# Performance work log

Hardware: AMD Instinct MI355X
Metric: run time of the kernel (lower is better)

## Reference

```python
import jax, jax.numpy as jnp
import numpy as np

B, N, D, H = 2, 2048, 512, 8
HD = D // H
EPS = 1e-5


def layernorm(x, g, b):
    m = jnp.mean(x, axis=-1, keepdims=True)
    v = jnp.var(x, axis=-1, keepdims=True)
    return (x - m) * jax.lax.rsqrt(v + EPS) * g + b


def setup_inputs() -> dict:
    key = jax.random.key(0)
    ks = jax.random.split(key, 16)
    s = 1.0 / np.sqrt(D)
    def lin(k, din, dout):
        k1, k2 = jax.random.split(k)
        return (jax.random.uniform(k1, (din, dout), jnp.float32, -s, s),
                jax.random.uniform(k2, (dout,), jnp.float32, -s, s))
    Wq, bq = lin(ks[0], D, D)
    Wk, bk = lin(ks[1], D, D)
    Wv, bv = lin(ks[2], D, D)
    Wo, bo = lin(ks[3], D, D)
    W1, b1 = lin(ks[4], D, 2 * D)
    W2, b2 = lin(ks[5], 2 * D, D)
    return {
        'y': jax.random.normal(ks[6], (B, N, D), jnp.float32),
        'Wq': Wq, 'bq': bq, 'Wk': Wk, 'bk': bk, 'Wv': Wv, 'bv': bv,
        'Wo': Wo, 'bo': bo,
        'ln1_g': jnp.ones((D,)), 'ln1_b': jnp.zeros((D,)),
        'ln2_g': jnp.ones((D,)), 'ln2_b': jnp.zeros((D,)),
        'W1': W1, 'b1': b1, 'W2': W2, 'b2': b2,
    }


def reference(y, Wq, bq, Wk, bk, Wv, bv, Wo, bo, ln1_g, ln1_b, ln2_g, ln2_b, W1, b1, W2, b2):
    x = layernorm(y, ln1_g, ln1_b)
    def heads(W, b):
        return (x @ W + b).reshape(B, N, H, HD).transpose(0, 2, 1, 3)  # bhnc
    q = heads(Wq, bq)
    k = heads(Wk, bk)
    v = heads(Wv, bv)
    score = jax.nn.softmax(jnp.einsum('bhic,bhjc->bhij', q, k) / np.sqrt(HD), axis=-1)
    r = jnp.einsum('bhij,bhjc->bhic', score, v)
    r = r.transpose(0, 2, 1, 3).reshape(B, N, D) @ Wo + bo
    y = y + r
    h = layernorm(y, ln2_g, ln2_b)
    h = jax.nn.gelu(h @ W1 + b1, approximate=False) @ W2 + b2
    return y + h
```

## Files before the change

kernel.cpp:

```cpp
#include <hip/hip_runtime.h>

#define DEVI __device__ __forceinline__

typedef unsigned short u16;
typedef unsigned int   u32;
typedef unsigned long long u64;
typedef float  f32x4  __attribute__((ext_vector_type(4)));
typedef __bf16 bf16x8 __attribute__((ext_vector_type(8)));

union FragU { bf16x8 b; u64 u[2]; __bf16 e[8]; };

DEVI u16 f2b(float x) { __bf16 t = (__bf16)x; return __builtin_bit_cast(u16, t); }

DEVI float exp2a(float x) { float r; asm("v_exp_f32 %0, %1" : "=v"(r) : "v"(x)); return r; }

DEVI void gload16(const void* g, void* l) {
  __builtin_amdgcn_global_load_lds((const __attribute__((address_space(1))) u32*)g,
                                   (__attribute__((address_space(3))) u32*)l, 16, 0, 0);
}

DEVI int kperm(int b) {
  return (b & 0x47) | ((b & 0x18) << 1) | ((b & 0x20) >> 2);
}
DEVI int swzo(int row, int b) {
  const int p = kperm(b);
  return ((((p >> 4) ^ row) & 7) << 4) | (p & 15);
}
DEVI FragU ldfrag(const char* base, int row, int g) {
  return *reinterpret_cast<const FragU*>(base + row * 128 + (((g ^ (row & 7)) << 4)));
}
DEVI FragU ldfrag64(const char* base, int row, int g) {
  return *reinterpret_cast<const FragU*>(base + row * 64 + (((g ^ (row & 3)) << 4)));
}
DEVI size_t gaddr(int row, int kbyte, int rowbytes) {
  return (size_t)row * rowbytes + (size_t)((kbyte & ~127) + swzo(row, kbyte & 127));
}

__global__ __launch_bounds__(256)
void prep(const float* __restrict__ Wq, const float* __restrict__ Wk,
          const float* __restrict__ Wv, const float* __restrict__ Wo,
          const float* __restrict__ W1, const float* __restrict__ W2,
          u16* __restrict__ wqkvT, u16* __restrict__ woT,
          u16* __restrict__ w1T, u16* __restrict__ w2T,
          const float* __restrict__ y, const float* __restrict__ ln1g,
          const float* __restrict__ ln1b, char* __restrict__ xb) {
  const int id = blockIdx.x;
  if (id < 2048) {
    __shared__ float tile[32][33];
    const float* src; u16* dst; int K, N, bx, by;
    if (id < 1024) {
      const int m = id >> 8, t = id & 255;
      K = 512; N = 512; bx = t & 15; by = t >> 4;
      src = (m == 0) ? Wq : (m == 1) ? Wk : (m == 2) ? Wv : Wo;
      dst = (m == 3) ? woT : wqkvT + m * 512 * 512;
    } else if (id < 1536) {
      const int t = id - 1024; K = 512; N = 1024; bx = t & 31; by = t >> 5;
      src = W1; dst = w1T;
    } else {
      const int t = id - 1536; K = 1024; N = 512; bx = t & 15; by = t >> 4;
      src = W2; dst = w2T;
    }
    const int tx = threadIdx.x & 31, ty = threadIdx.x >> 5;
#pragma unroll
    for (int i = 0; i < 4; ++i)
      tile[ty + i * 8][tx] = src[(size_t)(by * 32 + ty + i * 8) * N + bx * 32 + tx];
    __syncthreads();
    const int nl = threadIdx.x >> 3, kq = threadIdx.x & 7;
    const int n = bx * 32 + nl;
    const int kg = by * 32 + kq * 4;
    union { ushort4 s; u64 q; } pk;
    pk.s.x = f2b(tile[kq * 4 + 0][nl]);
    pk.s.y = f2b(tile[kq * 4 + 1][nl]);
    pk.s.z = f2b(tile[kq * 4 + 2][nl]);
    pk.s.w = f2b(tile[kq * 4 + 3][nl]);
    *(u64*)((char*)dst + gaddr(n, 2 * kg, 2 * K)) = pk.q;
  } else {
    const int row = id - 2048;
    const int t = threadIdx.x;
    const float2 v = ((const float2*)(y + (size_t)row * 512))[t];
    float s1 = v.x + v.y, s2 = v.x * v.x + v.y * v.y;
#pragma unroll
    for (int off = 32; off; off >>= 1) { s1 += __shfl_xor(s1, off); s2 += __shfl_xor(s2, off); }
    __shared__ float a1[4], a2[4];
    const int w = t >> 6;
    if ((t & 63) == 0) { a1[w] = s1; a2[w] = s2; }
    __syncthreads();
    s1 = a1[0] + a1[1] + a1[2] + a1[3];
    s2 = a2[0] + a2[1] + a2[2] + a2[3];
    const float mean = s1 * (1.f / 512.f);
    const float var = s2 * (1.f / 512.f) - mean * mean;
    const float rstd = rsqrtf(var + 1e-5f);
    const float2 gg = ((const float2*)ln1g)[t];
    const float2 bb = ((const float2*)ln1b)[t];
    const u16 o0 = f2b((v.x - mean) * rstd * gg.x + bb.x);
    const u16 o1 = f2b((v.y - mean) * rstd * gg.y + bb.y);
    *(u32*)(xb + gaddr(row, 4 * t, 1024)) = (u32)o0 | ((u32)o1 << 16);
  }
}

__global__ __launch_bounds__(256)
void ln_bf16(const float* __restrict__ x, const float* __restrict__ g,
             const float* __restrict__ b, char* __restrict__ out) {
  const int row = blockIdx.x;
  const int t = threadIdx.x;
  const float2 v = ((const float2*)(x + (size_t)row * 512))[t];
  float s1 = v.x + v.y, s2 = v.x * v.x + v.y * v.y;
#pragma unroll
  for (int off = 32; off; off >>= 1) { s1 += __shfl_xor(s1, off); s2 += __shfl_xor(s2, off); }
  __shared__ float a1[4], a2[4];
  const int w = t >> 6;
  if ((t & 63) == 0) { a1[w] = s1; a2[w] = s2; }
  __syncthreads();
  s1 = a1[0] + a1[1] + a1[2] + a1[3];
  s2 = a2[0] + a2[1] + a2[2] + a2[3];
  const float mean = s1 * (1.f / 512.f);
  const float var = s2 * (1.f / 512.f) - mean * mean;
  const float rstd = rsqrtf(var + 1e-5f);
  const float2 gg = ((const float2*)g)[t];
  const float2 bb = ((const float2*)b)[t];
  const u16 o0 = f2b((v.x - mean) * rstd * gg.x + bb.x);
  const u16 o1 = f2b((v.y - mean) * rstd * gg.y + bb.y);
  *(u32*)(out + gaddr(row, 4 * t, 1024)) = (u32)o0 | ((u32)o1 << 16);
}

enum { EPI_QKV = 0, EPI_RES = 1, EPI_GELU = 2 };

template <int EPI, int WM, int WN, int AM, int AN>
__global__ __launch_bounds__(WM * WN * 64)
void gemm_bf16(const char* __restrict__ A, const char* __restrict__ Bt, int N, int K,
               const float* __restrict__ bias,
               const float* __restrict__ bq, const float* __restrict__ bk,
               const float* __restrict__ bv,
               const float* __restrict__ res, float* __restrict__ outF,
               char* __restrict__ outB,
               u16* __restrict__ qo, char* __restrict__ ko, char* __restrict__ vo) {
  constexpr int NW = WM * WN;
  constexpr int TM = WM * AM * 16, TN = WN * AN * 16;
  constexpr int NCHA = TM / 8, NCHB = TN / 8, NCH = NCHA + NCHB;
  constexpr int CPW = NCH / NW;
  static_assert(CPW * NW == NCH, "chunk split");
  __shared__ __align__(16) char sA[2][TM * 128];
  __shared__ __align__(16) char sB[2][TN * 128];
  const int tid = threadIdx.x;
  const int l = tid & 63, w = tid >> 6;
  const int tm = blockIdx.x, tn = blockIdx.y;
  const int wr = w / WN, wc = w % WN;
  const int u = l >> 4, r16 = l & 15;
  const int lrow = l >> 3, lgr = l & 7;
  f32x4 acc[AM][AN] = {};
  const size_t KB = (size_t)K * 2;
  const char* Ab = A + (size_t)(tm * TM) * KB;
  const char* Bb = Bt + (size_t)(tn * TN) * KB;
  const int nkt = K >> 6;
  auto stage = [&](int buf, int kt) {
#pragma unroll
    for (int i = 0; i < CPW; ++i) {
      const int c = w * CPW + i;
      if (c < NCHA) {
        gload16(Ab + (size_t)(c * 8 + lrow) * KB + (size_t)kt * 128 + (lgr << 4),
                sA[buf] + c * 1024);
      } else {
        const int c2 = c - NCHA;
        gload16(Bb + (size_t)(c2 * 8 + lrow) * KB + (size_t)kt * 128 + (lgr << 4),
                sB[buf] + c2 * 1024);
      }
    }
  };
  stage(0, 0);
  int cur = 0;
  for (int kt = 0; kt < nkt; ++kt) {
    __syncthreads();
    if (kt + 1 < nkt) stage(cur ^ 1, kt + 1);
    __builtin_amdgcn_s_setprio(1);
#pragma unroll
    for (int ks = 0; ks < 2; ++ks) {
      FragU af[AM], bfr[AN];
      const int g = ks * 4 + u;
#pragma unroll
      for (int i = 0; i < AM; ++i)
        af[i] = ldfrag(sA[cur], wr * (AM * 16) + i * 16 + r16, g);
#pragma unroll
      for (int i = 0; i < AN; ++i)
        bfr[i] = ldfrag(sB[cur], wc * (AN * 16) + i * 16 + r16, g);
#pragma unroll
      for (int mi = 0; mi < AM; ++mi)
#pragma unroll
        for (int ni = 0; ni < AN; ++ni)
          acc[mi][ni] = __builtin_amdgcn_mfma_f32_16x16x32_bf16(af[mi].b, bfr[ni].b,
                                                                acc[mi][ni], 0, 0, 0);
    }
    __builtin_amdgcn_s_setprio(0);
    cur ^= 1;
  }
  const int row0 = tm * TM + wr * (AM * 16) + (u << 2);
  const int col0 = tn * TN + wc * (AN * 16) + r16;
#pragma unroll
  for (int mi = 0; mi < AM; ++mi) {
#pragma unroll
    for (int ni = 0; ni < AN; ++ni) {
      const int col = col0 + ni * 16;
      if (EPI == EPI_RES) {
#pragma unroll
        for (int r = 0; r < 4; ++r) {
          const int row = row0 + mi * 16 + r;
          outF[(size_t)row * N + col] = acc[mi][ni][r] + bias[col] + res[(size_t)row * N + col];
        }
      } else if (EPI == EPI_GELU) {
#pragma unroll
        for (int r = 0; r < 4; ++r) {
          const int row = row0 + mi * 16 + r;
          const float x = acc[mi][ni][r] + bias[col];
          *(u16*)(outB + gaddr(row, 2 * col, 2 * N)) =
              f2b(0.5f * x * (1.f + erff(x * 0.70710678118f)));
        }
      } else {
        const int which = col >> 9, cc = col & 511;
        const int h = cc >> 6, hd = cc & 63;
        if (which == 2) {
          const int rowa = row0 + mi * 16;
          const int bb2 = rowa >> 11, nt0 = rowa & 2047;
          const int bh = bb2 * 8 + h;
          const float bvv = bv[cc];
          union { ushort4 s; u64 q; } pk;
          pk.s.x = f2b(acc[mi][ni][0] + bvv);
          pk.s.y = f2b(acc[mi][ni][1] + bvv);
          pk.s.z = f2b(acc[mi][ni][2] + bvv);
          pk.s.w = f2b(acc[mi][ni][3] + bvv);
          const int kl = nt0 & 31;
          const int off64 = ((((kl >> 2) & 3) ^ (hd & 3)) << 4) | (((kl >> 4) & 1) << 3);
          *(u64*)(vo + (size_t)bh * 262144 + (size_t)(nt0 >> 5) * 4096 + hd * 64 + off64) = pk.q;
        } else {
#pragma unroll
          for (int r = 0; r < 4; ++r) {
            const int row = row0 + mi * 16 + r;
            const int bb2 = row >> 11, nt = row & 2047;
            const int bh = bb2 * 8 + h;
            if (which == 0)
              qo[((size_t)bh * 2048 + nt) * 64 + hd] = f2b((acc[mi][ni][r] + bq[cc]) * 0.18033688f);
            else
              *(u16*)(ko + (size_t)bh * 262144 + (size_t)(nt >> 6) * 8192 +
                      gaddr(nt & 63, 2 * hd, 128)) = f2b(acc[mi][ni][r] + bk[cc]);
          }
        }
      }
    }
  }
}

__global__ __launch_bounds__(512, 4)
void attn_k(const u16* __restrict__ q, const char* __restrict__ kswz,
            const char* __restrict__ vswz, char* __restrict__ r_out) {
  __shared__ __align__(16) char smem[65536];
  char (*sK)[2][4096] = (char(*)[2][4096])smem;
  char (*sV)[2][4096] = (char(*)[2][4096])(smem + 32768);
  const int tid = threadIdx.x;
  const int l = tid & 63, w = tid >> 6;
  const int kvh = w & 3, qw = w >> 2;
  const int bh = blockIdx.x, qt = blockIdx.y;
  const int u = l >> 4, r16 = l & 15;
  const char* kp = kswz + (size_t)bh * 262144;
  const char* vp = vswz + (size_t)bh * 262144;
  auto stage = [&](int buf, int i) {
    const int t32 = kvh * 16 + i;
    const size_t koff = (size_t)(t32 >> 1) * 8192 + (size_t)(t32 & 1) * 4096;
    const size_t voff = (size_t)t32 * 4096;
#pragma unroll
    for (int c = 0; c < 2; ++c) {
      gload16(kp + koff + qw * 2048 + c * 1024 + l * 16, sK[kvh][buf] + qw * 2048 + c * 1024);
      gload16(vp + voff + qw * 2048 + c * 1024 + l * 16, sV[kvh][buf] + qw * 2048 + c * 1024);
    }
  };
  stage(0, 0);
  FragU qf[2][2], ones;
  {
#pragma unroll
    for (int f = 0; f < 2; ++f) {
      const u16* qr = q + (size_t)bh * (2048 * 64) +
                      (size_t)(qt * 64 + qw * 32 + f * 16 + r16) * 64 + (u << 2);
      qf[f][0].u[0] = *(const u64*)qr;        qf[f][0].u[1] = *(const u64*)(qr + 16);
      qf[f][1].u[0] = *(const u64*)(qr + 32); qf[f][1].u[1] = *(const u64*)(qr + 48);
    }
    ones.u[0] = 0x3F803F803F803F80ull;
    ones.u[1] = 0x3F803F803F803F80ull;
  }
  f32x4 o[4][2] = {};
  f32x4 lacc[2] = {};
  int cur = 0;
  for (int i = 0; i < 16; ++i) {
    __syncthreads();
    if (i < 15) stage(cur ^ 1, i + 1);
    f32x4 st[2][2] = {};
    __builtin_amdgcn_s_setprio(1);
#pragma unroll
    for (int ks = 0; ks < 2; ++ks) {
      const int g = ks * 4 + u;
#pragma unroll
      for (int mi = 0; mi < 2; ++mi) {
        const FragU kf = ldfrag(sK[kvh][cur], mi * 16 + r16, g);
#pragma unroll
        for (int f = 0; f < 2; ++f)
          st[mi][f] = __builtin_amdgcn_mfma_f32_16x16x32_bf16(kf.b, qf[f][ks].b,
                                                              st[mi][f], 0, 0, 0);
      }
    }
    __builtin_amdgcn_s_setprio(0);
#pragma unroll
    for (int mi = 0; mi < 2; ++mi)
#pragma unroll
      for (int f = 0; f < 2; ++f)
#pragma unroll
        for (int r = 0; r < 4; ++r) st[mi][f][r] = exp2a(st[mi][f][r]);
    FragU pb[2];
#pragma unroll
    for (int f = 0; f < 2; ++f)
#pragma unroll
      for (int j = 0; j < 4; ++j) {
        pb[f].e[j]     = (__bf16)st[0][f][j];
        pb[f].e[j + 4] = (__bf16)st[1][f][j];
      }
    __builtin_amdgcn_s_setprio(1);
#pragma unroll
    for (int f = 0; f < 2; ++f)
      lacc[f] = __builtin_amdgcn_mfma_f32_16x16x32_bf16(ones.b, pb[f].b, lacc[f], 0, 0, 0);
#pragma unroll
    for (int mo = 0; mo < 4; ++mo) {
      const FragU vf = ldfrag64(sV[kvh][cur], mo * 16 + r16, u);
#pragma unroll
      for (int f = 0; f < 2; ++f)
        o[mo][f] = __builtin_amdgcn_mfma_f32_16x16x32_bf16(vf.b, pb[f].b, o[mo][f], 0, 0, 0);
    }
    __builtin_amdgcn_s_setprio(0);
    cur ^= 1;
  }
  __syncthreads();
  float* scrO = (float*)smem;
  float* scrL = (float*)smem + 12288;
  if (kvh != 0) {
    const int base = ((kvh - 1) * 2 + qw) * 2048;
    if (u == 0)
#pragma unroll
      for (int f = 0; f < 2; ++f)
        scrL[((kvh - 1) * 2 + qw) * 32 + f * 16 + r16] = lacc[f][0];
#pragma unroll
    for (int mo = 0; mo < 4; ++mo)
#pragma unroll
      for (int f = 0; f < 2; ++f)
#pragma unroll
        for (int r = 0; r < 4; ++r)
          scrO[base + (mo * 16 + u * 4 + r) * 32 + f * 16 + r16] = o[mo][f][r];
  }
  __syncthreads();
  if (kvh == 0) {
    const int h = bh & 7;
#pragma unroll
    for (int f = 0; f < 2; ++f) {
      float lsum = lacc[f][0];
#pragma unroll
      for (int g2 = 0; g2 < 3; ++g2)
        lsum += scrL[(g2 * 2 + qw) * 32 + f * 16 + r16];
      const float linv = 1.f / lsum;
      const int tok = (bh >> 3) * 2048 + qt * 64 + qw * 32 + f * 16 + r16;
#pragma unroll
      for (int mo = 0; mo < 4; ++mo) {
        union { ushort4 s; u64 qq; } pk;
        float vv[4];
#pragma unroll
        for (int r = 0; r < 4; ++r) {
          float acc2 = o[mo][f][r];
#pragma unroll
          for (int g2 = 0; g2 < 3; ++g2)
            acc2 += scrO[(g2 * 2 + qw) * 2048 + (mo * 16 + u * 4 + r) * 32 + f * 16 + r16];
          vv[r] = acc2 * linv;
        }
        pk.s.x = f2b(vv[0]); pk.s.y = f2b(vv[1]); pk.s.z = f2b(vv[2]); pk.s.w = f2b(vv[3]);
        *(u64*)(r_out + (size_t)tok * 1024 + h * 128 + swzo(tok, mo * 32 + (u << 3))) = pk.qq;
      }
    }
  }
}

extern "C" void kernel_launch(void* const* d_in, const int* in_sizes, int n_in,
                              void* d_out, int out_size, void* d_ws, size_t ws_size,
                              hipStream_t stream) {
  const float* y    = (const float*)d_in[0];
  const float* Wq   = (const float*)d_in[1];
  const float* bq   = (const float*)d_in[2];
  const float* Wk   = (const float*)d_in[3];
  const float* bk   = (const float*)d_in[4];
  const float* Wv   = (const float*)d_in[5];
  const float* bv   = (const float*)d_in[6];
  const float* Wo   = (const float*)d_in[7];
  const float* bo   = (const float*)d_in[8];
  const float* ln1g = (const float*)d_in[9];
  const float* ln1b = (const float*)d_in[10];
  const float* ln2g = (const float*)d_in[11];
  const float* ln2b = (const float*)d_in[12];
  const float* W1   = (const float*)d_in[13];
  const float* b1   = (const float*)d_in[14];
  const float* W2   = (const float*)d_in[15];
  const float* b2   = (const float*)d_in[16];
  float* out = (float*)d_out;
  char* ws = (char*)d_ws;
  char* xb    = ws;
  u16*  qb    = (u16*)(ws + (4u << 20));
  char* kswz  = ws + (8u << 20);
  char* vswz  = ws + (12u << 20);
  char* rb    = ws + (16u << 20);
  char* g1b   = ws + (20u << 20);
  u16* wqkvT  = (u16*)(ws + (28u << 20));
  u16* woT    = wqkvT + 1536 * 512;
  u16* w1T    = woT + 512 * 512;
  u16* w2T    = w1T + 1024 * 512;

  prep<<<6144, 256, 0, stream>>>(Wq, Wk, Wv, Wo, W1, W2, wqkvT, woT, w1T, w2T,
                                 y, ln1g, ln1b, xb);
  gemm_bf16<EPI_QKV, 2, 2, 4, 2><<<dim3(32, 24), 256, 0, stream>>>(
      xb, (const char*)wqkvT, 1536, 512, nullptr, bq, bk, bv,
      nullptr, nullptr, nullptr, qb, kswz, vswz);
  attn_k<<<dim3(16, 32), 512, 0, stream>>>(qb, kswz, vswz, rb);
  gemm_bf16<EPI_RES, 2, 2, 2, 2><<<dim3(64, 8), 256, 0, stream>>>(
      rb, (const char*)woT, 512, 512, bo, nullptr, nullptr, nullptr,
      y, out, nullptr, nullptr, nullptr, nullptr);
  ln_bf16<<<4096, 256, 0, stream>>>(out, ln2g, ln2b, xb);
  gemm_bf16<EPI_GELU, 2, 2, 4, 2><<<dim3(32, 16), 256, 0, stream>>>(
      xb, (const char*)w1T, 1024, 512, b1, nullptr, nullptr, nullptr,
      nullptr, nullptr, g1b, nullptr, nullptr, nullptr);
  gemm_bf16<EPI_RES, 2, 2, 2, 2><<<dim3(64, 8), 256, 0, stream>>>(
      g1b, (const char*)w2T, 512, 1024, b2, nullptr, nullptr, nullptr,
      out, out, nullptr, nullptr, nullptr, nullptr);
}
```

Before: 90.68 us.

## Fold LayerNorm2 into Wo epilogue and W1 GEMM via algebraic rewrite

Removes the standalone ln_bf16 kernel. The Wo GEMM epilogue now writes the raw residual both as fp32 and bf16, and accumulates per-row sum and sum-of-squares into a stats buffer with atomics. The W1 GEMM applies the normalization afterwards: ln2 gamma is folded into W1 during prep, and column vectors gamma·W1 and beta·W1 are precomputed. This saves a launch and a full pass over the activations, at the cost of atomics, extra precomputation in prep, and lower precision because the un-normalized residual is quantized to bf16 before normalization.

```diff
diff --git a/kernel.cpp b/kernel.cpp
--- a/kernel.cpp
+++ b/kernel.cpp
@@ -43,40 +43,45 @@
           u16* __restrict__ wqkvT, u16* __restrict__ woT,
           u16* __restrict__ w1T, u16* __restrict__ w2T,
           const float* __restrict__ y, const float* __restrict__ ln1g,
-          const float* __restrict__ ln1b, char* __restrict__ xb) {
+          const float* __restrict__ ln1b, char* __restrict__ xb,
+          const float* __restrict__ ln2g, const float* __restrict__ ln2b,
+          float* __restrict__ u1, float* __restrict__ v1, float* __restrict__ stat) {
   const int id = blockIdx.x;
+  const int t = threadIdx.x;
   if (id < 2048) {
     __shared__ float tile[32][33];
     const float* src; u16* dst; int K, N, bx, by;
+    bool fold = false;
     if (id < 1024) {
-      const int m = id >> 8, t = id & 255;
-      K = 512; N = 512; bx = t & 15; by = t >> 4;
+      const int m = id >> 8, tt = id & 255;
+      K = 512; N = 512; bx = tt & 15; by = tt >> 4;
       src = (m == 0) ? Wq : (m == 1) ? Wk : (m == 2) ? Wv : Wo;
       dst = (m == 3) ? woT : wqkvT + m * 512 * 512;
     } else if (id < 1536) {
-      const int t = id - 1024; K = 512; N = 1024; bx = t & 31; by = t >> 5;
-      src = W1; dst = w1T;
+      const int tt = id - 1024; K = 512; N = 1024; bx = tt & 31; by = tt >> 5;
+      src = W1; dst = w1T; fold = true;
     } else {
-      const int t = id - 1536; K = 1024; N = 512; bx = t & 15; by = t >> 4;
+      const int tt = id - 1536; K = 1024; N = 512; bx = tt & 15; by = tt >> 4;
       src = W2; dst = w2T;
     }
-    const int tx = threadIdx.x & 31, ty = threadIdx.x >> 5;
+    const int tx = t & 31, ty = t >> 5;
 #pragma unroll
     for (int i = 0; i < 4; ++i)
       tile[ty + i * 8][tx] = src[(size_t)(by * 32 + ty + i * 8) * N + bx * 32 + tx];
     __syncthreads();
-    const int nl = threadIdx.x >> 3, kq = threadIdx.x & 7;
+    const int nl = t >> 3, kq = t & 7;
     const int n = bx * 32 + nl;
     const int kg = by * 32 + kq * 4;
     union { ushort4 s; u64 q; } pk;
-    pk.s.x = f2b(tile[kq * 4 + 0][nl]);
-    pk.s.y = f2b(tile[kq * 4 + 1][nl]);
-    pk.s.z = f2b(tile[kq * 4 + 2][nl]);
-    pk.s.w = f2b(tile[kq * 4 + 3][nl]);
+    float e0 = tile[kq * 4 + 0][nl], e1 = tile[kq * 4 + 1][nl];
+    float e2 = tile[kq * 4 + 2][nl], e3 = tile[kq * 4 + 3][nl];
+    if (fold) {
+      e0 *= ln2g[kg + 0]; e1 *= ln2g[kg + 1]; e2 *= ln2g[kg + 2]; e3 *= ln2g[kg + 3];
+    }
+    pk.s.x = f2b(e0); pk.s.y = f2b(e1); pk.s.z = f2b(e2); pk.s.w = f2b(e3);
     *(u64*)((char*)dst + gaddr(n, 2 * kg, 2 * K)) = pk.q;
-  } else {
+  } else if (id < 6144) {
     const int row = id - 2048;
-    const int t = threadIdx.x;
     const float2 v = ((const float2*)(y + (size_t)row * 512))[t];
     float s1 = v.x + v.y, s2 = v.x * v.x + v.y * v.y;
 #pragma unroll
@@ -95,35 +100,32 @@
     const u16 o0 = f2b((v.x - mean) * rstd * gg.x + bb.x);
     const u16 o1 = f2b((v.y - mean) * rstd * gg.y + bb.y);
     *(u32*)(xb + gaddr(row, 4 * t, 1024)) = (u32)o0 | ((u32)o1 << 16);
-  }
-}
-
-__global__ __launch_bounds__(256)
-void ln_bf16(const float* __restrict__ x, const float* __restrict__ g,
-             const float* __restrict__ b, char* __restrict__ out) {
-  const int row = blockIdx.x;
-  const int t = threadIdx.x;
-  const float2 v = ((const float2*)(x + (size_t)row * 512))[t];
-  float s1 = v.x + v.y, s2 = v.x * v.x + v.y * v.y;
-#pragma unroll
-  for (int off = 32; off; off >>= 1) { s1 += __shfl_xor(s1, off); s2 += __shfl_xor(s2, off); }
-  __shared__ float a1[4], a2[4];
-  const int w = t >> 6;
-  if ((t & 63) == 0) { a1[w] = s1; a2[w] = s2; }
-  __syncthreads();
-  s1 = a1[0] + a1[1] + a1[2] + a1[3];
-  s2 = a2[0] + a2[1] + a2[2] + a2[3];
-  const float mean = s1 * (1.f / 512.f);
-  const float var = s2 * (1.f / 512.f) - mean * mean;
-  const float rstd = rsqrtf(var + 1e-5f);
-  const float2 gg = ((const float2*)g)[t];
-  const float2 bb = ((const float2*)b)[t];
-  const u16 o0 = f2b((v.x - mean) * rstd * gg.x + bb.x);
-  const u16 o1 = f2b((v.y - mean) * rstd * gg.y + bb.y);
-  *(u32*)(out + gaddr(row, 4 * t, 1024)) = (u32)o0 | ((u32)o1 << 16);
-}
-
-enum { EPI_QKV = 0, EPI_RES = 1, EPI_GELU = 2 };
+  } else if (id < 6176) {
+    __shared__ float red2[2][8][33];
+    const int base = (id - 6144) * 32;
+    const int j = base + (t & 31), rg = t >> 5;
+    float su = 0.f, sv = 0.f;
+    for (int k = rg; k < 512; k += 8) {
+      const float wv = W1[(size_t)k * 1024 + j];
+      su += ln2g[k] * wv;
+      sv += ln2b[k] * wv;
+    }
+    red2[0][rg][t & 31] = su;
+    red2[1][rg][t & 31] = sv;
+    __syncthreads();
+    if (t < 32) {
+      float a = 0.f, b = 0.f;
+#pragma unroll
+      for (int g2 = 0; g2 < 8; ++g2) { a += red2[0][g2][t]; b += red2[1][g2][t]; }
+      u1[base + t] = a;
+      v1[base + t] = b;
+    }
+  } else {
+    for (int i = t; i < 8192; i += 256) stat[i] = 0.f;
+  }
+}
+
+enum { EPI_QKV = 0, EPI_RES = 1, EPI_GELU = 2, EPI_RESLN = 3 };
 
 template <int EPI, int WM, int WN, int AM, int AN>
 __global__ __launch_bounds__(WM * WN * 64)
@@ -133,7 +135,9 @@
                const float* __restrict__ bv,
                const float* __restrict__ res, float* __restrict__ outF,
                char* __restrict__ outB,
-               u16* __restrict__ qo, char* __restrict__ ko, char* __restrict__ vo) {
+               u16* __restrict__ qo, char* __restrict__ ko, char* __restrict__ vo,
+               float* __restrict__ stat, const float* __restrict__ u1,
+               const float* __restrict__ v1) {
   constexpr int NW = WM * WN;
   constexpr int TM = WM * AM * 16, TN = WN * AN * 16;
   constexpr int NCHA = TM / 8, NCHB = TN / 8, NCH = NCHA + NCHB;
@@ -194,6 +198,75 @@
   }
   const int row0 = tm * TM + wr * (AM * 16) + (u << 2);
   const int col0 = tn * TN + wc * (AN * 16) + r16;
+  if (EPI == EPI_GELU) {
+    float mrow[AM][4], rrow[AM][4];
+#pragma unroll
+    for (int mi = 0; mi < AM; ++mi)
+#pragma unroll
+      for (int r = 0; r < 4; ++r) {
+        const int row = row0 + mi * 16 + r;
+        const float2 st = ((const float2*)stat)[row];
+        const float m = st.x * (1.f / 512.f);
+        const float var = st.y * (1.f / 512.f) - m * m;
+        rrow[mi][r] = rsqrtf(var + 1e-5f);
+        mrow[mi][r] = m;
+      }
+#pragma unroll
+    for (int mi = 0; mi < AM; ++mi) {
+#pragma unroll
+      for (int ni = 0; ni < AN; ++ni) {
+        const int col = col0 + ni * 16;
+        const float uu = u1[col], vv = v1[col], bb = bias[col];
+#pragma unroll
+        for (int r = 0; r < 4; ++r) {
+          const int row = row0 + mi * 16 + r;
+          const float z = rrow[mi][r] * (acc[mi][ni][r] - mrow[mi][r] * uu) + vv + bb;
+          *(u16*)(outB + gaddr(row, 2 * col, 2 * N)) =
+              f2b(0.5f * z * (1.f + erff(z * 0.70710678118f)));
+        }
+      }
+    }
+    return;
+  }
+  if (EPI == EPI_RESLN) {
+    float s1l[AM][4] = {}, s2l[AM][4] = {};
+#pragma unroll
+    for (int mi = 0; mi < AM; ++mi) {
+#pragma unroll
+      for (int ni = 0; ni < AN; ++ni) {
+        const int col = col0 + ni * 16;
+#pragma unroll
+        for (int r = 0; r < 4; ++r) {
+          const int row = row0 + mi * 16 + r;
+          const float v = acc[mi][ni][r] + bias[col] + res[(size_t)row * N + col];
+          outF[(size_t)row * N + col] = v;
+          *(u16*)(outB + gaddr(row, 2 * col, 1024)) = f2b(v);
+          s1l[mi][r] += v;
+          s2l[mi][r] += v * v;
+        }
+      }
+    }
+#pragma unroll
+    for (int off = 1; off < 16; off <<= 1)
+#pragma unroll
+      for (int mi = 0; mi < AM; ++mi)
+#pragma unroll
+        for (int r = 0; r < 4; ++r) {
+          s1l[mi][r] += __shfl_xor(s1l[mi][r], off);
+          s2l[mi][r] += __shfl_xor(s2l[mi][r], off);
+        }
+    if (r16 == 0) {
+#pragma unroll
+      for (int mi = 0; mi < AM; ++mi)
+#pragma unroll
+        for (int r = 0; r < 4; ++r) {
+          const int row = row0 + mi * 16 + r;
+          atomicAdd(&stat[2 * row], s1l[mi][r]);
+          atomicAdd(&stat[2 * row + 1], s2l[mi][r]);
+        }
+    }
+    return;
+  }
 #pragma unroll
   for (int mi = 0; mi < AM; ++mi) {
 #pragma unroll
@@ -204,14 +277,6 @@
         for (int r = 0; r < 4; ++r) {
           const int row = row0 + mi * 16 + r;
           outF[(size_t)row * N + col] = acc[mi][ni][r] + bias[col] + res[(size_t)row * N + col];
-        }
-      } else if (EPI == EPI_GELU) {
-#pragma unroll
-        for (int r = 0; r < 4; ++r) {
-          const int row = row0 + mi * 16 + r;
-          const float x = acc[mi][ni][r] + bias[col];
-          *(u16*)(outB + gaddr(row, 2 * col, 2 * N)) =
-              f2b(0.5f * x * (1.f + erff(x * 0.70710678118f)));
         }
       } else {
         const int which = col >> 9, cc = col & 511;
@@ -411,21 +476,23 @@
   u16* woT    = wqkvT + 1536 * 512;
   u16* w1T    = woT + 512 * 512;
   u16* w2T    = w1T + 1024 * 512;
-
-  prep<<<6144, 256, 0, stream>>>(Wq, Wk, Wv, Wo, W1, W2, wqkvT, woT, w1T, w2T,
-                                 y, ln1g, ln1b, xb);
+  float* statb = (float*)(ws + (33u << 20));
+  float* u1b   = statb + 8192;
+  float* v1b   = u1b + 1024;
+
+  prep<<<6177, 256, 0, stream>>>(Wq, Wk, Wv, Wo, W1, W2, wqkvT, woT, w1T, w2T,
+                                 y, ln1g, ln1b, xb, ln2g, ln2b, u1b, v1b, statb);
   gemm_bf16<EPI_QKV, 2, 2, 4, 2><<<dim3(32, 24), 256, 0, stream>>>(
       xb, (const char*)wqkvT, 1536, 512, nullptr, bq, bk, bv,
-      nullptr, nullptr, nullptr, qb, kswz, vswz);
+      nullptr, nullptr, nullptr, qb, kswz, vswz, nullptr, nullptr, nullptr);
   attn_k<<<dim3(16, 32), 512, 0, stream>>>(qb, kswz, vswz, rb);
-  gemm_bf16<EPI_RES, 2, 2, 2, 2><<<dim3(64, 8), 256, 0, stream>>>(
+  gemm_bf16<EPI_RESLN, 2, 2, 2, 2><<<dim3(64, 8), 256, 0, stream>>>(
       rb, (const char*)woT, 512, 512, bo, nullptr, nullptr, nullptr,
-      y, out, nullptr, nullptr, nullptr, nullptr);
-  ln_bf16<<<4096, 256, 0, stream>>>(out, ln2g, ln2b, xb);
+      y, out, xb, nullptr, nullptr, nullptr, statb, nullptr, nullptr);
   gemm_bf16<EPI_GELU, 2, 2, 4, 2><<<dim3(32, 16), 256, 0, stream>>>(
       xb, (const char*)w1T, 1024, 512, b1, nullptr, nullptr, nullptr,
-      nullptr, nullptr, g1b, nullptr, nullptr, nullptr);
+      nullptr, nullptr, g1b, nullptr, nullptr, nullptr, statb, u1b, v1b);
   gemm_bf16<EPI_RES, 2, 2, 2, 2><<<dim3(64, 8), 256, 0, stream>>>(
       g1b, (const char*)w2T, 512, 1024, b2, nullptr, nullptr, nullptr,
-      out, out, nullptr, nullptr, nullptr, nullptr);
-}
+      out, out, nullptr, nullptr, nullptr, nullptr, nullptr, nullptr, nullptr);
+}
```

Result: slower. 100.2 us (+10.5%).
